# Kernel tuning notes

Measured on AMD Instinct MI355X. Metric: run time of the kernel, lower is better.

Reference implementation:

```python
import jax, jax.numpy as jnp
import numpy as np

N_HEADS = 8
ROPE_BASE = 10000.0


def _rope(x, pos):
    # x: (BN, T, H, D); pos: (T,)
    D = x.shape[-1]
    inv_freq = 1.0 / (ROPE_BASE ** (jnp.arange(0, D, 2, dtype=jnp.float32) / D))  # (D/2,)
    ang = pos[:, None].astype(jnp.float32) * inv_freq[None, :]                    # (T, D/2)
    cos = jnp.concatenate([jnp.cos(ang), jnp.cos(ang)], axis=-1)[None, :, None, :]  # (1,T,1,D)
    sin = jnp.concatenate([jnp.sin(ang), jnp.sin(ang)], axis=-1)[None, :, None, :]
    x1, x2 = x[..., : D // 2], x[..., D // 2 :]
    rot = jnp.concatenate([-x2, x1], axis=-1)
    return x * cos + rot * sin


def setup_inputs() -> dict:
    key = jax.random.key(0)
    ks = jax.random.split(key, 5)
    B, T, N, E = 2, 1024, 4, 256
    s = 1.0 / np.sqrt(E)
    return {
        "input_tensor": jax.random.normal(ks[0], (B, T, N, E), dtype=jnp.float32),
        "w_attn": jax.random.normal(ks[1], (E, 3 * E), dtype=jnp.float32) * s,
        "b_attn": jnp.zeros((3 * E,), dtype=jnp.float32),
        "w_proj": jax.random.normal(ks[2], (E, E), dtype=jnp.float32) * s,
        "b_proj": jnp.zeros((E,), dtype=jnp.float32),
    }


def reference(input_tensor, w_attn, b_attn, w_proj, b_proj):
    B, T, N, E = input_tensor.shape
    H = N_HEADS
    D = E // H
    # (B,T,N,E) -> (B*N, T, E)
    x = jnp.transpose(input_tensor, (0, 2, 1, 3)).reshape(B * N, T, E)
    qkv = x @ w_attn + b_attn  # (BN, T, 3E)
    q, k, v = jnp.split(qkv, 3, axis=-1)
    q = q.reshape(B * N, T, H, D)
    k = k.reshape(B * N, T, H, D)
    v = v.reshape(B * N, T, H, D)
    pos = jnp.arange(T)
    q = _rope(q, pos)
    k = _rope(k, pos)
    # causal SDPA
    scale = 1.0 / jnp.sqrt(jnp.asarray(D, dtype=q.dtype))
    scores = jnp.einsum("bthd,bshd->bhts", q, k) * scale  # (BN,H,T,T)
    causal = jnp.tril(jnp.ones((T, T), dtype=bool))
    scores = jnp.where(causal[None, None], scores, jnp.finfo(scores.dtype).min)
    probs = jax.nn.softmax(scores, axis=-1)
    out = jnp.einsum("bhts,bshd->bthd", probs, v).reshape(B * N, T, E)
    out = out @ w_proj + b_proj
    # (BN,T,E) -> (B,T,N,E)
    return jnp.transpose(out.reshape(B, N, T, E), (0, 2, 1, 3))
```

## Files before the change

### kernel.cpp

```cpp
#include <hip/hip_runtime.h>
#include <hip/hip_bf16.h>

#define T_ 1024
#define NB 4
#define E_ 256
#define H_ 8
#define D_ 32
#define E3 768

typedef __attribute__((ext_vector_type(4))) short v4s;
typedef __attribute__((ext_vector_type(8))) short v8s;
typedef __attribute__((ext_vector_type(4))) float v4f;

#define EXP2F(x) __builtin_amdgcn_exp2f(x)

__device__ __forceinline__ unsigned short f2bf(float x) {
    union { float f; unsigned int u; } v; v.f = x;
    unsigned int r = v.u + 0x7fffu + ((v.u >> 16) & 1u);
    return (unsigned short)(r >> 16);
}
__device__ __forceinline__ unsigned int pack2(float lo, float hi) {
    return (unsigned int)f2bf(lo) | ((unsigned int)f2bf(hi) << 16);
}

__global__ __launch_bounds__(256) void prep_kernel(
    const float* __restrict__ w_attn, const float* __restrict__ w_proj,
    const float* __restrict__ x,
    unsigned short* __restrict__ WT, unsigned short* __restrict__ WPT,
    unsigned short* __restrict__ xb,
    float* __restrict__ ctab, float* __restrict__ stab)
{
    const int blk = blockIdx.x;
    if (blk < 256) {
        __shared__ float tile[32][33];
        const int bx = blk & 31, by = blk >> 5;
        const float* src; unsigned short* dst; int N, n0;
        if (bx < 24) { src = w_attn; dst = WT;  N = 768; n0 = bx * 32; }
        else         { src = w_proj; dst = WPT; N = 256; n0 = (bx - 24) * 32; }
        const int k0 = by * 32;
        const int xx = threadIdx.x & 31, y4 = (threadIdx.x >> 5) * 4;
        #pragma unroll
        for (int i = 0; i < 4; ++i)
            tile[y4 + i][xx] = src[(size_t)(k0 + y4 + i) * N + n0 + xx];
        __syncthreads();
        #pragma unroll
        for (int i = 0; i < 4; ++i)
            dst[(size_t)(n0 + y4 + i) * 256 + k0 + xx] = f2bf(tile[xx][y4 + i]);
    } else if (blk < 768) {
        const size_t i = (size_t)(blk - 256) * 4096 + threadIdx.x * 16;
        #pragma unroll
        for (int j = 0; j < 4; ++j) {
            float4 v = *(const float4*)(x + i + j * 4);
            ushort4 o;
            o.x = f2bf(v.x); o.y = f2bf(v.y); o.z = f2bf(v.z); o.w = f2bf(v.w);
            *(ushort4*)(xb + i + j * 4) = o;
        }
    } else {
        const int idx = (blk - 768) * 256 + threadIdx.x;
        const int t = idx >> 4, jj = idx & 15;
        const float invf = __expf(-(float)jj * 0.5756462732485115f);
        float s, c;
        sincosf((float)t * invf, &s, &c);
        ctab[idx] = c;
        stab[idx] = s;
    }
}

__global__ __launch_bounds__(256) void qkv_mfma_kernel(
    const unsigned short* __restrict__ xb,
    const float* __restrict__ b_attn,
    const unsigned short* __restrict__ WT,
    const float* __restrict__ ctab, const float* __restrict__ stab,
    unsigned short* __restrict__ Qb, unsigned short* __restrict__ Kb,
    unsigned short* __restrict__ VW)
{
    const int tid  = threadIdx.x;
    const int wsb  = tid >> 6;
    const int lane = tid & 63;
    const int g = lane >> 4, c = lane & 15;
    const int m0 = blockIdx.x * 64 + wsb * 16;
    const int n0 = blockIdx.y * 64;
    const int bn = m0 >> 10;
    const int b  = bn >> 2, nidx = bn & 3;
    const int t_base = m0 & 1023;

    const unsigned short* xrow = xb + ((size_t)(b * T_ + t_base + c) * NB + nidx) * E_;

    v4f acc[4];
    #pragma unroll
    for (int tt = 0; tt < 4; ++tt) acc[tt] = (v4f){0.f, 0.f, 0.f, 0.f};

    #pragma unroll
    for (int k0 = 0; k0 < 256; k0 += 32) {
        v8s afrag = *(const v8s*)(xrow + k0 + 8 * g);
        #pragma unroll
        for (int tt = 0; tt < 4; ++tt) {
            v8s bfrag = *(const v8s*)(WT + (size_t)(n0 + tt * 16 + c) * 256 + k0 + 8 * g);
            acc[tt] = __builtin_amdgcn_mfma_f32_16x16x32_bf16(afrag, bfrag, acc[tt], 0, 0, 0);
        }
    }

    float bias[4];
    #pragma unroll
    for (int tt = 0; tt < 4; ++tt) bias[tt] = b_attn[n0 + tt * 16 + c];

    const int type = n0 >> 8;
    const int nl0  = n0 & 255;

    if (type <= 1) {
        unsigned short* Dst = (type == 0) ? Qb : Kb;
        float sn[4], cs[4];
        #pragma unroll
        for (int r = 0; r < 4; ++r) {
            const int ti = (t_base + 4 * g + r) * 16 + c;
            cs[r] = ctab[ti];
            sn[r] = stab[ti];
        }
        #pragma unroll
        for (int tt = 0; tt < 4; ++tt) {
            const int n_l = nl0 + tt * 16;
            const int h = n_l >> 5, d = (n_l & 31) + c;
            const int bh = bn * 8 + h;
            const float sgn = (tt & 1) ? 1.f : -1.f;
            const int  ptt = tt ^ 1;
            #pragma unroll
            for (int r = 0; r < 4; ++r) {
                float v0 = acc[tt][r] + bias[tt];
                float v1 = acc[ptt][r] + bias[ptt];
                float o  = v0 * cs[r] + sgn * v1 * sn[r];
                int   t  = t_base + 4 * g + r;
                Dst[((size_t)bh * T_ + t) * D_ + d] = f2bf(o);
            }
        }
    } else {
        const int wv_ = t_base >> 5;
        const int tw  = (t_base & 31) + 4 * g;
        #pragma unroll
        for (int tt = 0; tt < 4; ++tt) {
            const int n_l = nl0 + tt * 16;
            const int h = n_l >> 5, d = (n_l & 31) + c;
            const int bh = bn * 8 + h;
            ushort4 pk;
            pk.x = f2bf(acc[tt][0] + bias[tt]);
            pk.y = f2bf(acc[tt][1] + bias[tt]);
            pk.z = f2bf(acc[tt][2] + bias[tt]);
            pk.w = f2bf(acc[tt][3] + bias[tt]);
            *(ushort4*)(VW + (((size_t)bh * 32 + wv_) * 32 + d) * 32 + tw) = pk;
        }
    }
}

#define KMUL   0.2550343f
#define SHIFTL 11.5415603f

__global__ __launch_bounds__(256) void attn_kernel(
    const unsigned short* __restrict__ Qb,
    const unsigned short* __restrict__ Kb,
    const unsigned short* __restrict__ VW,
    unsigned short* __restrict__ Ob)
{
    const int tid  = threadIdx.x;
    const int wv   = tid >> 6;
    const int lane = tid & 63;
    const int g = lane >> 4, c = lane & 15;
    const int bx = blockIdx.x;
    const int bh = bx & 63;
    const int k  = bx >> 6;

    const int qts[2] = { k + 8 * wv, k + 56 - 8 * wv };
    const int lim0 = qts[0] >> 1;
    const int lim1 = qts[1] >> 1;

    v8s qf[2];
    #pragma unroll
    for (int j = 0; j < 2; ++j)
        qf[j] = *(const v8s*)(Qb + ((size_t)bh * T_ + qts[j] * 16 + c) * D_ + 8 * g);

    v4f o0[2], o1[2];
    float ll[2];
    #pragma unroll
    for (int j = 0; j < 2; ++j) {
        o0[j] = (v4f){0.f, 0.f, 0.f, 0.f};
        o1[j] = (v4f){0.f, 0.f, 0.f, 0.f};
        ll[j] = 0.f;
    }

    const unsigned short* Ksrc = Kb + (size_t)bh * T_ * D_;
    const unsigned short* Vsrc = VW + (size_t)bh * 32 * 1024;

    const int koff = c * 32 + 8 * g;
    const int voff = c * 32 + 4 * g;

    v8s kA_n = *(const v8s*)(Ksrc + koff);
    v8s kB_n = *(const v8s*)(Ksrc + 512 + koff);
    v4s va0_n = *(const v4s*)(Vsrc + voff);
    v4s vb0_n = *(const v4s*)(Vsrc + voff + 16);
    v4s va1_n = *(const v4s*)(Vsrc + 512 + voff);
    v4s vb1_n = *(const v4s*)(Vsrc + 512 + voff + 16);

    for (int w = 0; w <= lim1; ++w) {
        v8s kfA = kA_n, kfB = kB_n;
        v4s va0 = va0_n, vb0 = vb0_n, va1 = va1_n, vb1 = vb1_n;
        if (w < lim1) {
            const unsigned short* kp = Ksrc + (size_t)(w + 1) * 1024;
            const unsigned short* vp = Vsrc + (size_t)(w + 1) * 1024;
            kA_n = *(const v8s*)(kp + koff);
            kB_n = *(const v8s*)(kp + 512 + koff);
            va0_n = *(const v4s*)(vp + voff);
            vb0_n = *(const v4s*)(vp + voff + 16);
            va1_n = *(const v4s*)(vp + 512 + voff);
            vb1_n = *(const v4s*)(vp + 512 + voff + 16);
        }

        v8s vf0, vf1;
        #pragma unroll
        for (int i = 0; i < 4; ++i) {
            vf0[i] = va0[i]; vf0[4 + i] = vb0[i];
            vf1[i] = va1[i]; vf1[4 + i] = vb1[i];
        }

        const int s0 = w * 32;
        #pragma unroll
        for (int j = 0; j < 2; ++j) {
            const int qt  = qts[j];
            const int lim = qt >> 1;
            if (lim < w) continue;
            const int q = qt * 16 + c;

            v4f zero = {0.f, 0.f, 0.f, 0.f};
            v4f sA = __builtin_amdgcn_mfma_f32_16x16x32_bf16(kfA, qf[j], zero, 0, 0, 0);
            v4f sB = __builtin_amdgcn_mfma_f32_16x16x32_bf16(kfB, qf[j], zero, 0, 0, 0);

            const bool diag = (lim == w);
            float p[8];
            #pragma unroll
            for (int r = 0; r < 4; ++r) {
                float pa = EXP2F(fmaf(sA[r], KMUL, -SHIFTL));
                float pb = EXP2F(fmaf(sB[r], KMUL, -SHIFTL));
                if (diag) {
                    if (s0 + 4 * g + r > q)      pa = 0.f;
                    if (s0 + 16 + 4 * g + r > q) pb = 0.f;
                }
                p[r] = pa; p[4 + r] = pb;
                ll[j] += pa + pb;
            }
            union { v8s v; uint4 u; } pu;
            pu.u.x = pack2(p[0], p[1]);
            pu.u.y = pack2(p[2], p[3]);
            pu.u.z = pack2(p[4], p[5]);
            pu.u.w = pack2(p[6], p[7]);
            o0[j] = __builtin_amdgcn_mfma_f32_16x16x32_bf16(pu.v, vf0, o0[j], 0, 0, 0);
            o1[j] = __builtin_amdgcn_mfma_f32_16x16x32_bf16(pu.v, vf1, o1[j], 0, 0, 0);
        }
    }

    const int bn = bh >> 3, h = bh & 7;
    #pragma unroll
    for (int j = 0; j < 2; ++j) {
        float l_s = ll[j];
        l_s += __shfl_xor(l_s, 16, 64);
        l_s += __shfl_xor(l_s, 32, 64);
        float linv = 1.0f / l_s;
        float lr[4];
        #pragma unroll
        for (int r = 0; r < 4; ++r) lr[r] = __shfl(linv, 4 * g + r, 64);
        const int q0 = qts[j] * 16;
        #pragma unroll
        for (int r = 0; r < 4; ++r) {
            unsigned short* Orow = Ob + ((size_t)bn * T_ + q0 + 4 * g + r) * E_ + h * D_;
            Orow[c]      = f2bf(o0[j][r] * lr[r]);
            Orow[16 + c] = f2bf(o1[j][r] * lr[r]);
        }
    }
}

__global__ __launch_bounds__(256) void proj_mfma_kernel(
    const unsigned short* __restrict__ Ob,
    const unsigned short* __restrict__ WPT,
    const float* __restrict__ b_proj,
    float* __restrict__ out)
{
    const int tid  = threadIdx.x;
    const int wsb  = tid >> 6;
    const int lane = tid & 63;
    const int g = lane >> 4, c = lane & 15;
    const int m0 = blockIdx.x * 64 + wsb * 16;
    const int n0 = blockIdx.y * 64;
    const int bn = m0 >> 10;
    const int b  = bn >> 2, nidx = bn & 3;
    const int t_base = m0 & 1023;

    const unsigned short* arow = Ob + ((size_t)bn * T_ + t_base + c) * E_;

    v4f acc[4];
    #pragma unroll
    for (int tt = 0; tt < 4; ++tt) acc[tt] = (v4f){0.f, 0.f, 0.f, 0.f};

    #pragma unroll
    for (int s = 0; s < 8; ++s) {
        v8s afrag = *(const v8s*)(arow + s * 32 + 8 * g);
        #pragma unroll
        for (int tt = 0; tt < 4; ++tt) {
            v8s bfrag = *(const v8s*)(WPT + (size_t)(n0 + tt * 16 + c) * 256 + s * 32 + 8 * g);
            acc[tt] = __builtin_amdgcn_mfma_f32_16x16x32_bf16(afrag, bfrag, acc[tt], 0, 0, 0);
        }
    }

    #pragma unroll
    for (int tt = 0; tt < 4; ++tt) {
        const int n = n0 + tt * 16 + c;
        const float bp = b_proj[n];
        #pragma unroll
        for (int r = 0; r < 4; ++r) {
            const int t = t_base + 4 * g + r;
            out[((size_t)(b * T_ + t) * NB + nidx) * E_ + n] = acc[tt][r] + bp;
        }
    }
}

extern "C" void kernel_launch(void* const* d_in, const int* in_sizes, int n_in,
                              void* d_out, int out_size, void* d_ws, size_t ws_size,
                              hipStream_t stream)
{
    const float* x      = (const float*)d_in[0];
    const float* w_attn = (const float*)d_in[1];
    const float* b_attn = (const float*)d_in[2];
    const float* w_proj = (const float*)d_in[3];
    const float* b_proj = (const float*)d_in[4];
    float* out = (float*)d_out;

    unsigned short* Qb  = (unsigned short*)d_ws;
    unsigned short* Kb  = Qb + 2097152;
    unsigned short* VW  = Kb + 2097152;
    unsigned short* Ob  = VW + 2097152;
    unsigned short* xb  = Ob + 2097152;
    unsigned short* WT  = xb + 2097152;
    unsigned short* WPT = WT + 196608;
    float* ctab = (float*)(WPT + 65536);
    float* stab = ctab + 16384;

    prep_kernel<<<832, 256, 0, stream>>>(w_attn, w_proj, x, WT, WPT, xb, ctab, stab);
    qkv_mfma_kernel<<<dim3(128, 12), 256, 0, stream>>>(xb, b_attn, WT, ctab, stab, Qb, Kb, VW);
    attn_kernel<<<512, 256, 0, stream>>>(Qb, Kb, VW, Ob);
    proj_mfma_kernel<<<dim3(128, 4), 256, 0, stream>>>(Ob, WPT, b_proj, out);
}
```

Baseline: 133.4 us.

## Fuse x bf16 conversion into QKV GEMM, permute V layout, use hardware bf16 pack

Removes the separate fp32→bf16 conversion of the input from the prep kernel. The QKV GEMM now reads fp32 x directly and converts it in registers with v_cvt_pk_bf16_f32. V is stored in a permuted layout so the attention kernel loads each V fragment with one 16-byte load instead of two 8-byte loads plus a register shuffle. P packing also switches to the hardware convert instruction. The trade-off is that the QKV kernel reads x as fp32, twice the bytes, and reloads it for each of the 12 column-block tiles.

```diff
diff --git a/kernel.cpp b/kernel.cpp
--- a/kernel.cpp
+++ b/kernel.cpp
@@ -19,15 +19,15 @@
     unsigned int r = v.u + 0x7fffu + ((v.u >> 16) & 1u);
     return (unsigned short)(r >> 16);
 }
-__device__ __forceinline__ unsigned int pack2(float lo, float hi) {
-    return (unsigned int)f2bf(lo) | ((unsigned int)f2bf(hi) << 16);
+__device__ __forceinline__ unsigned int cvtpk(float lo, float hi) {
+    unsigned int r;
+    asm("v_cvt_pk_bf16_f32 %0, %1, %2" : "=v"(r) : "v"(lo), "v"(hi));
+    return r;
 }
 
 __global__ __launch_bounds__(256) void prep_kernel(
     const float* __restrict__ w_attn, const float* __restrict__ w_proj,
-    const float* __restrict__ x,
     unsigned short* __restrict__ WT, unsigned short* __restrict__ WPT,
-    unsigned short* __restrict__ xb,
     float* __restrict__ ctab, float* __restrict__ stab)
 {
     const int blk = blockIdx.x;
@@ -46,17 +46,8 @@
         #pragma unroll
         for (int i = 0; i < 4; ++i)
             dst[(size_t)(n0 + y4 + i) * 256 + k0 + xx] = f2bf(tile[xx][y4 + i]);
-    } else if (blk < 768) {
-        const size_t i = (size_t)(blk - 256) * 4096 + threadIdx.x * 16;
-        #pragma unroll
-        for (int j = 0; j < 4; ++j) {
-            float4 v = *(const float4*)(x + i + j * 4);
-            ushort4 o;
-            o.x = f2bf(v.x); o.y = f2bf(v.y); o.z = f2bf(v.z); o.w = f2bf(v.w);
-            *(ushort4*)(xb + i + j * 4) = o;
-        }
     } else {
-        const int idx = (blk - 768) * 256 + threadIdx.x;
+        const int idx = (blk - 256) * 256 + threadIdx.x;
         const int t = idx >> 4, jj = idx & 15;
         const float invf = __expf(-(float)jj * 0.5756462732485115f);
         float s, c;
@@ -67,7 +58,7 @@
 }
 
 __global__ __launch_bounds__(256) void qkv_mfma_kernel(
-    const unsigned short* __restrict__ xb,
+    const float* __restrict__ x,
     const float* __restrict__ b_attn,
     const unsigned short* __restrict__ WT,
     const float* __restrict__ ctab, const float* __restrict__ stab,
@@ -84,7 +75,7 @@
     const int b  = bn >> 2, nidx = bn & 3;
     const int t_base = m0 & 1023;
 
-    const unsigned short* xrow = xb + ((size_t)(b * T_ + t_base + c) * NB + nidx) * E_;
+    const float* xrow = x + ((size_t)(b * T_ + t_base + c) * NB + nidx) * E_;
 
     v4f acc[4];
     #pragma unroll
@@ -92,11 +83,17 @@
 
     #pragma unroll
     for (int k0 = 0; k0 < 256; k0 += 32) {
-        v8s afrag = *(const v8s*)(xrow + k0 + 8 * g);
+        float4 f0 = *(const float4*)(xrow + k0 + 8 * g);
+        float4 f1 = *(const float4*)(xrow + k0 + 8 * g + 4);
+        union { v8s v; uint4 u; } af;
+        af.u.x = cvtpk(f0.x, f0.y);
+        af.u.y = cvtpk(f0.z, f0.w);
+        af.u.z = cvtpk(f1.x, f1.y);
+        af.u.w = cvtpk(f1.z, f1.w);
         #pragma unroll
         for (int tt = 0; tt < 4; ++tt) {
             v8s bfrag = *(const v8s*)(WT + (size_t)(n0 + tt * 16 + c) * 256 + k0 + 8 * g);
-            acc[tt] = __builtin_amdgcn_mfma_f32_16x16x32_bf16(afrag, bfrag, acc[tt], 0, 0, 0);
+            acc[tt] = __builtin_amdgcn_mfma_f32_16x16x32_bf16(af.v, bfrag, acc[tt], 0, 0, 0);
         }
     }
 
@@ -135,6 +132,7 @@
     } else {
         const int wv_ = t_base >> 5;
         const int tw  = (t_base & 31) + 4 * g;
+        const int pos0 = ((tw >> 4) & 1) * 4 + ((tw >> 2) & 3) * 8;
         #pragma unroll
         for (int tt = 0; tt < 4; ++tt) {
             const int n_l = nl0 + tt * 16;
@@ -145,7 +143,7 @@
             pk.y = f2bf(acc[tt][1] + bias[tt]);
             pk.z = f2bf(acc[tt][2] + bias[tt]);
             pk.w = f2bf(acc[tt][3] + bias[tt]);
-            *(ushort4*)(VW + (((size_t)bh * 32 + wv_) * 32 + d) * 32 + tw) = pk;
+            *(ushort4*)(VW + (((size_t)bh * 32 + wv_) * 32 + d) * 32 + pos0) = pk;
         }
     }
 }
@@ -168,7 +166,6 @@
     const int k  = bx >> 6;
 
     const int qts[2] = { k + 8 * wv, k + 56 - 8 * wv };
-    const int lim0 = qts[0] >> 1;
     const int lim1 = qts[1] >> 1;
 
     v8s qf[2];
@@ -189,34 +186,23 @@
     const unsigned short* Vsrc = VW + (size_t)bh * 32 * 1024;
 
     const int koff = c * 32 + 8 * g;
-    const int voff = c * 32 + 4 * g;
-
-    v8s kA_n = *(const v8s*)(Ksrc + koff);
-    v8s kB_n = *(const v8s*)(Ksrc + 512 + koff);
-    v4s va0_n = *(const v4s*)(Vsrc + voff);
-    v4s vb0_n = *(const v4s*)(Vsrc + voff + 16);
-    v4s va1_n = *(const v4s*)(Vsrc + 512 + voff);
-    v4s vb1_n = *(const v4s*)(Vsrc + 512 + voff + 16);
+    const int voff = c * 32 + 8 * g;
+
+    v8s kA_n  = *(const v8s*)(Ksrc + koff);
+    v8s kB_n  = *(const v8s*)(Ksrc + 512 + koff);
+    v8s vf0_n = *(const v8s*)(Vsrc + voff);
+    v8s vf1_n = *(const v8s*)(Vsrc + 512 + voff);
 
     for (int w = 0; w <= lim1; ++w) {
         v8s kfA = kA_n, kfB = kB_n;
-        v4s va0 = va0_n, vb0 = vb0_n, va1 = va1_n, vb1 = vb1_n;
+        v8s vf0 = vf0_n, vf1 = vf1_n;
         if (w < lim1) {
             const unsigned short* kp = Ksrc + (size_t)(w + 1) * 1024;
             const unsigned short* vp = Vsrc + (size_t)(w + 1) * 1024;
-            kA_n = *(const v8s*)(kp + koff);
-            kB_n = *(const v8s*)(kp + 512 + koff);
-            va0_n = *(const v4s*)(vp + voff);
-            vb0_n = *(const v4s*)(vp + voff + 16);
-            va1_n = *(const v4s*)(vp + 512 + voff);
-            vb1_n = *(const v4s*)(vp + 512 + voff + 16);
-        }
-
-        v8s vf0, vf1;
-        #pragma unroll
-        for (int i = 0; i < 4; ++i) {
-            vf0[i] = va0[i]; vf0[4 + i] = vb0[i];
-            vf1[i] = va1[i]; vf1[4 + i] = vb1[i];
+            kA_n  = *(const v8s*)(kp + koff);
+            kB_n  = *(const v8s*)(kp + 512 + koff);
+            vf0_n = *(const v8s*)(vp + voff);
+            vf1_n = *(const v8s*)(vp + 512 + voff);
         }
 
         const int s0 = w * 32;
@@ -245,10 +231,10 @@
                 ll[j] += pa + pb;
             }
             union { v8s v; uint4 u; } pu;
-            pu.u.x = pack2(p[0], p[1]);
-            pu.u.y = pack2(p[2], p[3]);
-            pu.u.z = pack2(p[4], p[5]);
-            pu.u.w = pack2(p[6], p[7]);
+            pu.u.x = cvtpk(p[0], p[1]);
+            pu.u.y = cvtpk(p[2], p[3]);
+            pu.u.z = cvtpk(p[4], p[5]);
+            pu.u.w = cvtpk(p[6], p[7]);
             o0[j] = __builtin_amdgcn_mfma_f32_16x16x32_bf16(pu.v, vf0, o0[j], 0, 0, 0);
             o1[j] = __builtin_amdgcn_mfma_f32_16x16x32_bf16(pu.v, vf1, o1[j], 0, 0, 0);
         }
@@ -333,14 +319,13 @@
     unsigned short* Kb  = Qb + 2097152;
     unsigned short* VW  = Kb + 2097152;
     unsigned short* Ob  = VW + 2097152;
-    unsigned short* xb  = Ob + 2097152;
-    unsigned short* WT  = xb + 2097152;
+    unsigned short* WT  = Ob + 2097152;
     unsigned short* WPT = WT + 196608;
     float* ctab = (float*)(WPT + 65536);
     float* stab = ctab + 16384;
 
-    prep_kernel<<<832, 256, 0, stream>>>(w_attn, w_proj, x, WT, WPT, xb, ctab, stab);
-    qkv_mfma_kernel<<<dim3(128, 12), 256, 0, stream>>>(xb, b_attn, WT, ctab, stab, Qb, Kb, VW);
+    prep_kernel<<<320, 256, 0, stream>>>(w_attn, w_proj, WT, WPT, ctab, stab);
+    qkv_mfma_kernel<<<dim3(128, 12), 256, 0, stream>>>(x, b_attn, WT, ctab, stab, Qb, Kb, VW);
     attn_kernel<<<512, 256, 0, stream>>>(Qb, Kb, VW, Ob);
     proj_mfma_kernel<<<dim3(128, 4), 256, 0, stream>>>(Ob, WPT, b_proj, out);
 }
```

Measured after the change: 131.2 us. Within noise of the previous version (-1.7%).
